# Performance work log

Measured on AMD Instinct MI355X. Metric: run time of the kernel, lower is better.

Reference implementation:

```python
import jax, jax.numpy as jnp
import numpy as np

B, T, I, H, C = 8192, 784, 1, 30, 10


def setup_inputs() -> dict:
    key = jax.random.key(0)
    ks = jax.random.split(key, 7)
    s_ih = 1.0 / np.sqrt(H)
    return {
        "x": jax.random.normal(ks[0], (B, T, I), dtype=jnp.float32),
        "W_ih": jax.random.uniform(ks[1], (H, I), jnp.float32, -s_ih, s_ih),
        "W_hh": jax.random.uniform(ks[2], (H, H), jnp.float32, -s_ih, s_ih),
        "b_ih": jax.random.uniform(ks[3], (H,), jnp.float32, -s_ih, s_ih),
        "b_hh": jax.random.uniform(ks[4], (H,), jnp.float32, -s_ih, s_ih),
        "W_fc": jax.random.uniform(ks[5], (C, H), jnp.float32, -s_ih, s_ih),
        "b_fc": jax.random.uniform(ks[6], (C,), jnp.float32, -s_ih, s_ih),
    }


def reference(x, W_ih, W_hh, b_ih, b_hh, W_fc, b_fc):
    # x: [B, T, I] -> scan over time. h_t = tanh(x_t W_ih^T + b_ih + h W_hh^T + b_hh)
    xs = jnp.swapaxes(x, 0, 1)  # [T, B, I]
    h0 = jnp.zeros((x.shape[0], W_hh.shape[0]), dtype=x.dtype)
    bias = b_ih + b_hh  # [H]

    def step(h, xt):
        h_new = jnp.tanh(xt @ W_ih.T + h @ W_hh.T + bias)
        return h_new, None

    hT, _ = jax.lax.scan(step, h0, xs)  # hT: [B, H] == out[:, -1, :]
    return hT @ W_fc.T + b_fc  # [B, C]
```

## Files before the change

kernel.cpp:

```cpp
#include <hip/hip_runtime.h>


#define TT 784
#define HH 30
#define HP 32
#define CC 10
#define TPB 32
#define NB 8
#define LSTR 36

__global__ __launch_bounds__(256, 4)
void rnn_scan_kernel(const float* __restrict__ x,
                     const float* __restrict__ W_ih,
                     const float* __restrict__ W_hh,
                     const float* __restrict__ b_ih,
                     const float* __restrict__ b_hh,
                     const float* __restrict__ W_fc,
                     const float* __restrict__ b_fc,
                     float* __restrict__ out) {
    __shared__ float hbuf[NB * LSTR];

    const int tid = threadIdx.x;
    const int bl  = tid >> 5;
    const int r   = tid & 31;
    const int b   = blockIdx.x * NB + bl;

    float w[HP];
    const bool valid = (r < HH);
#pragma unroll
    for (int j = 0; j < HP; ++j)
        w[j] = (valid && (j < HH)) ? W_hh[r * HH + j] : 0.0f;
    const float bias = valid ? (b_ih[r] + b_hh[r]) : 0.0f;
    const float wih  = valid ? W_ih[r] : 0.0f;

    float* hp = &hbuf[bl * LSTR];
    hp[r] = 0.0f;
    __builtin_amdgcn_wave_barrier();

    const float* xb = x + (size_t)b * TT;
    float4 xq = *(const float4*)(xb);

    for (int q = 0; q < TT / 4; ++q) {
        float4 nxt = (q + 1 < TT / 4) ? *(const float4*)(xb + (q + 1) * 4)
                                      : make_float4(0.f, 0.f, 0.f, 0.f);
#pragma unroll
        for (int u = 0; u < 4; ++u) {
            const float xt = (u == 0) ? xq.x : (u == 1) ? xq.y
                           : (u == 2) ? xq.z : xq.w;
            float a0 = __builtin_fmaf(xt, wih, bias);
            float a1 = 0.0f;
#pragma unroll
            for (int jq = 0; jq < HP / 4; ++jq) {
                const float4 hq = *(const float4*)(hp + jq * 4);
                a0 = __builtin_fmaf(w[jq * 4 + 0], hq.x, a0);
                a1 = __builtin_fmaf(w[jq * 4 + 1], hq.y, a1);
                a0 = __builtin_fmaf(w[jq * 4 + 2], hq.z, a0);
                a1 = __builtin_fmaf(w[jq * 4 + 3], hq.w, a1);
            }
            const float acc = a0 + a1;
            const float e  = __builtin_exp2f(acc * 2.885390081777927f);
            const float hn = __builtin_fmaf(-2.0f,
                                 __builtin_amdgcn_rcpf(e + 1.0f), 1.0f);
            __builtin_amdgcn_wave_barrier();
            hp[r] = hn;
            __builtin_amdgcn_wave_barrier();
        }
        xq = nxt;
    }

    if (r < CC) {
        float acc = b_fc[r];
#pragma unroll
        for (int j = 0; j < HH; ++j)
            acc = __builtin_fmaf(W_fc[r * HH + j], hp[j], acc);
        out[(size_t)b * CC + r] = acc;
    }
}

extern "C" void kernel_launch(void* const* d_in, const int* in_sizes, int n_in,
                              void* d_out, int out_size, void* d_ws, size_t ws_size,
                              hipStream_t stream) {
    const float* x    = (const float*)d_in[0];
    const float* W_ih = (const float*)d_in[1];
    const float* W_hh = (const float*)d_in[2];
    const float* b_ih = (const float*)d_in[3];
    const float* b_hh = (const float*)d_in[4];
    const float* W_fc = (const float*)d_in[5];
    const float* b_fc = (const float*)d_in[6];

    hipLaunchKernelGGL(rnn_scan_kernel,
                       dim3(8192 / NB), dim3(NB * TPB), 0, stream,
                       x, W_ih, W_hh, b_ih, b_hh, W_fc, b_fc,
                       (float*)d_out);
}
```

Baseline: 334.5 us.

## Replace LDS hidden-state exchange with DPP row rotations, 16 lanes per sequence

Each sequence now maps to 16 lanes that each own two hidden units, and the shared-memory round trip per timestep is replaced by DPP row_ror rotations that broadcast hidden values across the 16-lane row. The recurrent weights are stored pre-rotated in registers to match. The goal is to remove LDS write/read latency and wave barriers from the serial recurrence and to pack 16 sequences per block. In exchange each lane does twice the FMAs, uses more registers (occupancy hint lowered to 2), and the per-step dependency chain gets longer.

```diff
diff --git a/kernel.cpp b/kernel.cpp
--- a/kernel.cpp
+++ b/kernel.cpp
@@ -3,13 +3,17 @@
 
 #define TT 784
 #define HH 30
-#define HP 32
 #define CC 10
-#define TPB 32
-#define NB 8
-#define LSTR 36
+#define TPB 16
+#define NB 16
 
-__global__ __launch_bounds__(256, 4)
+template<int CTRL>
+__device__ __forceinline__ float rotf(float v) {
+    return __int_as_float(__builtin_amdgcn_mov_dpp(
+        __float_as_int(v), CTRL, 0xf, 0xf, false));
+}
+
+__global__ __launch_bounds__(256, 2)
 void rnn_scan_kernel(const float* __restrict__ x,
                      const float* __restrict__ W_ih,
                      const float* __restrict__ W_hh,
@@ -18,27 +22,60 @@
                      const float* __restrict__ W_fc,
                      const float* __restrict__ b_fc,
                      float* __restrict__ out) {
-    __shared__ float hbuf[NB * LSTR];
+    __shared__ float hbuf[NB][34];
 
     const int tid = threadIdx.x;
-    const int bl  = tid >> 5;
-    const int r   = tid & 31;
+    const int bl  = tid >> 4;
+    const int r   = tid & 15;
     const int b   = blockIdx.x * NB + bl;
+    const int r2  = r + 16;
 
-    float w[HP];
-    const bool valid = (r < HH);
+    float wa[16], wb[16], wc[16], wd[16];
+    const bool v2 = (r2 < HH);
 #pragma unroll
-    for (int j = 0; j < HP; ++j)
-        w[j] = (valid && (j < HH)) ? W_hh[r * HH + j] : 0.0f;
-    const float bias = valid ? (b_ih[r] + b_hh[r]) : 0.0f;
-    const float wih  = valid ? W_ih[r] : 0.0f;
+    for (int k = 0; k < 16; ++k) {
+        const int j = (r - k) & 15;
+        const int c = 16 + j;
+        wa[k] = W_hh[r * HH + j];
+        wb[k] = (c < HH) ? W_hh[r * HH + c] : 0.0f;
+        wc[k] = v2 ? W_hh[r2 * HH + j] : 0.0f;
+        wd[k] = (v2 && c < HH) ? W_hh[r2 * HH + c] : 0.0f;
+    }
+    float bias0 = b_ih[r] + b_hh[r];
+    float wih0  = W_ih[r];
+    float bias1 = v2 ? (b_ih[r2] + b_hh[r2]) : 0.0f;
+    float wih1  = v2 ? W_ih[r2] : 0.0f;
 
-    float* hp = &hbuf[bl * LSTR];
-    hp[r] = 0.0f;
-    __builtin_amdgcn_wave_barrier();
+    asm volatile("" : "+v"(wa[0]), "+v"(wa[1]), "+v"(wa[2]),  "+v"(wa[3]),
+                      "+v"(wa[4]), "+v"(wa[5]), "+v"(wa[6]),  "+v"(wa[7]),
+                      "+v"(wa[8]), "+v"(wa[9]), "+v"(wa[10]), "+v"(wa[11]),
+                      "+v"(wa[12]),"+v"(wa[13]),"+v"(wa[14]), "+v"(wa[15]));
+    asm volatile("" : "+v"(wb[0]), "+v"(wb[1]), "+v"(wb[2]),  "+v"(wb[3]),
+                      "+v"(wb[4]), "+v"(wb[5]), "+v"(wb[6]),  "+v"(wb[7]),
+                      "+v"(wb[8]), "+v"(wb[9]), "+v"(wb[10]), "+v"(wb[11]),
+                      "+v"(wb[12]),"+v"(wb[13]),"+v"(wb[14]), "+v"(wb[15]));
+    asm volatile("" : "+v"(wc[0]), "+v"(wc[1]), "+v"(wc[2]),  "+v"(wc[3]),
+                      "+v"(wc[4]), "+v"(wc[5]), "+v"(wc[6]),  "+v"(wc[7]),
+                      "+v"(wc[8]), "+v"(wc[9]), "+v"(wc[10]), "+v"(wc[11]),
+                      "+v"(wc[12]),"+v"(wc[13]),"+v"(wc[14]), "+v"(wc[15]));
+    asm volatile("" : "+v"(wd[0]), "+v"(wd[1]), "+v"(wd[2]),  "+v"(wd[3]),
+                      "+v"(wd[4]), "+v"(wd[5]), "+v"(wd[6]),  "+v"(wd[7]),
+                      "+v"(wd[8]), "+v"(wd[9]), "+v"(wd[10]), "+v"(wd[11]),
+                      "+v"(wd[12]),"+v"(wd[13]),"+v"(wd[14]), "+v"(wd[15]));
+    asm volatile("" : "+v"(bias0), "+v"(wih0), "+v"(bias1), "+v"(wih1));
+
+    float h0 = 0.0f, h1 = 0.0f;
 
     const float* xb = x + (size_t)b * TT;
     float4 xq = *(const float4*)(xb);
+
+#define KSTEP(k) {                                          \
+        const float r0 = rotf<0x120 | (k)>(h0);             \
+        const float r1 = rotf<0x120 | (k)>(h1);             \
+        acc0 = __builtin_fmaf(wa[k], r0, acc0);             \
+        acc0 = __builtin_fmaf(wb[k], r1, acc0);             \
+        acc1 = __builtin_fmaf(wc[k], r0, acc1);             \
+        acc1 = __builtin_fmaf(wd[k], r1, acc1); }
 
     for (int q = 0; q < TT / 4; ++q) {
         float4 nxt = (q + 1 < TT / 4) ? *(const float4*)(xb + (q + 1) * 4)
@@ -47,32 +84,32 @@
         for (int u = 0; u < 4; ++u) {
             const float xt = (u == 0) ? xq.x : (u == 1) ? xq.y
                            : (u == 2) ? xq.z : xq.w;
-            float a0 = __builtin_fmaf(xt, wih, bias);
-            float a1 = 0.0f;
-#pragma unroll
-            for (int jq = 0; jq < HP / 4; ++jq) {
-                const float4 hq = *(const float4*)(hp + jq * 4);
-                a0 = __builtin_fmaf(w[jq * 4 + 0], hq.x, a0);
-                a1 = __builtin_fmaf(w[jq * 4 + 1], hq.y, a1);
-                a0 = __builtin_fmaf(w[jq * 4 + 2], hq.z, a0);
-                a1 = __builtin_fmaf(w[jq * 4 + 3], hq.w, a1);
-            }
-            const float acc = a0 + a1;
-            const float e  = __builtin_exp2f(acc * 2.885390081777927f);
-            const float hn = __builtin_fmaf(-2.0f,
-                                 __builtin_amdgcn_rcpf(e + 1.0f), 1.0f);
-            __builtin_amdgcn_wave_barrier();
-            hp[r] = hn;
-            __builtin_amdgcn_wave_barrier();
+            float acc0 = __builtin_fmaf(xt, wih0, bias0);
+            float acc1 = __builtin_fmaf(xt, wih1, bias1);
+            acc0 = __builtin_fmaf(wa[0], h0, acc0);
+            acc0 = __builtin_fmaf(wb[0], h1, acc0);
+            acc1 = __builtin_fmaf(wc[0], h0, acc1);
+            acc1 = __builtin_fmaf(wd[0], h1, acc1);
+            KSTEP(1)  KSTEP(2)  KSTEP(3)  KSTEP(4)  KSTEP(5)
+            KSTEP(6)  KSTEP(7)  KSTEP(8)  KSTEP(9)  KSTEP(10)
+            KSTEP(11) KSTEP(12) KSTEP(13) KSTEP(14) KSTEP(15)
+            const float e0 = __builtin_exp2f(acc0 * 2.885390081777927f);
+            const float e1 = __builtin_exp2f(acc1 * 2.885390081777927f);
+            h0 = __builtin_fmaf(-2.0f, __builtin_amdgcn_rcpf(e0 + 1.0f), 1.0f);
+            h1 = __builtin_fmaf(-2.0f, __builtin_amdgcn_rcpf(e1 + 1.0f), 1.0f);
         }
         xq = nxt;
     }
+#undef KSTEP
 
+    hbuf[bl][r]      = h0;
+    hbuf[bl][16 + r] = h1;
+    __builtin_amdgcn_wave_barrier();
     if (r < CC) {
         float acc = b_fc[r];
 #pragma unroll
         for (int j = 0; j < HH; ++j)
-            acc = __builtin_fmaf(W_fc[r * HH + j], hp[j], acc);
+            acc = __builtin_fmaf(W_fc[r * HH + j], hbuf[bl][j], acc);
         out[(size_t)b * CC + r] = acc;
     }
 }
```

After: 430.1 us. +28.6%, slower.
